# Kernel optimization log

Hardware: AMD Instinct MI355X
Metric: run time of the kernel (lower is better)

## Reference

```python
import jax, jax.numpy as jnp
import numpy as np

NUM_HEADS = 8
HEAD_DIM = 128
MAX_RES = 224.0


def rope_embed(feat_shape, dim, max_res=MAX_RES):
    # timm pixel_freq_bands: 2**linspace(0, log2(max_res)-1, dim//4) * pi
    num_bands = dim // 4
    bands = (2.0 ** jnp.linspace(0.0, float(np.log2(max_res)) - 1.0, num_bands)) * jnp.pi
    # pixel coords in [-1, 1] per spatial dim
    coords = [jnp.linspace(-1.0, 1.0, s) for s in feat_shape]
    grid = jnp.stack(jnp.meshgrid(*coords, indexing='ij'), axis=-1)[..., None]  # [H,W,2,1]
    pos = grid * bands  # [H,W,2,num_bands]
    n = int(np.prod(feat_shape))
    sin = jnp.repeat(jnp.sin(pos).reshape(n, -1), 2, axis=-1)  # [n, dim]
    cos = jnp.repeat(jnp.cos(pos).reshape(n, -1), 2, axis=-1)  # [n, dim]
    return sin, cos


def _rot(x):
    # interleaved rotate-half: (x0,x1,x2,x3,...) -> (-x1,x0,-x3,x2,...)
    return jnp.stack([-x[..., 1::2], x[..., ::2]], axis=-1).reshape(x.shape)


def setup_inputs() -> dict:
    key = jax.random.key(0)
    k1, k2, k3, k4 = jax.random.split(key, 4)
    C, E = 1024, 1024
    x = jax.random.normal(k1, (64, C, 16, 16), dtype=jnp.float32)
    qkv_w = jax.random.normal(k2, (3 * E, C), dtype=jnp.float32) * (C ** -0.5)
    qkv_b = jnp.zeros((3 * E,), dtype=jnp.float32)
    proj_w = jax.random.normal(k3, (E, E), dtype=jnp.float32) * (E ** -0.5)
    proj_b = jax.random.normal(k4, (E,), dtype=jnp.float32) * 0.02
    return {"x": x, "qkv_w": qkv_w, "qkv_b": qkv_b, "proj_w": proj_w, "proj_b": proj_b}


def reference(x, qkv_w, qkv_b, proj_w, proj_b):
    B, C, H, W = x.shape
    n = H * W
    scale = HEAD_DIM ** -0.5
    sin_emb, cos_emb = rope_embed((H, W), HEAD_DIM)  # [n, head_dim]

    t = x.reshape(B, C, n).transpose(0, 2, 1)                      # [B, n, C]
    t = jnp.concatenate([t.mean(axis=1, keepdims=True), t], axis=1)  # [B, n+1, C]

    qkv = t @ qkv_w.T + qkv_b                                      # [B, n+1, 3E]
    qkv = qkv.reshape(B, n + 1, 3, NUM_HEADS, HEAD_DIM).transpose(2, 0, 3, 1, 4)
    q, k, v = qkv[0], qkv[1], qkv[2]                               # [B, h, n+1, d]

    def apply_rope(z):
        zc, zs = z[:, :, :1], z[:, :, 1:]
        zs = zs * cos_emb + _rot(zs) * sin_emb
        return jnp.concatenate([zc, zs], axis=2)

    q = apply_rope(q)
    k = apply_rope(k)

    attn = jax.nn.softmax(jnp.einsum('bhqd,bhkd->bhqk', q, k) * scale, axis=-1)
    out = jnp.einsum('bhqk,bhkd->bhqd', attn, v)
    out = out.transpose(0, 2, 1, 3).reshape(B, n + 1, -1)           # [B, n+1, E]
    out = out @ proj_w.T + proj_b
    return out[:, 0]
```

## Files before the change

kernel.cpp:

```cpp
#include <hip/hip_runtime.h>
#include <math.h>

#define PI_F 3.14159265358979323846f
#define KSTEP 0.21959209425992272f

using bf16x8 = __attribute__((ext_vector_type(8))) short;
using f32x4 = __attribute__((ext_vector_type(4))) float;
using u16x8 = __attribute__((ext_vector_type(8))) unsigned short;

static __device__ __forceinline__ float wave_reduce_sum(float v) {
#pragma unroll
  for (int off = 32; off; off >>= 1) v += __shfl_down(v, off);
  return v;
}

static __device__ __forceinline__ unsigned short f2bf(float f) {
  unsigned u = __float_as_uint(f);
  return (unsigned short)((u + 0x7fffu + ((u >> 16) & 1u)) >> 16);
}

static __device__ __forceinline__ float bf2f(unsigned short s) {
  return __uint_as_float(((unsigned)s) << 16);
}

static __device__ __forceinline__ void gload_lds16(const void* g, void* l) {
  __builtin_amdgcn_global_load_lds((const __attribute__((address_space(1))) unsigned int*)g,
                                   (__attribute__((address_space(3))) unsigned int*)l, 16, 0, 0);
}

__global__ __launch_bounds__(256) void prep_kernel(const float* __restrict__ x,
                                                   const float* __restrict__ qkv_w,
                                                   unsigned short* __restrict__ xt,
                                                   float* __restrict__ t_mean,
                                                   unsigned short* __restrict__ wk_bf,
                                                   float2* __restrict__ sc) {
  const int bid = blockIdx.x;
  const int t = threadIdx.x;
  __shared__ float tile[64][33];
  if (bid < 1024) {
    const int ct = bid & 15, b = bid >> 4;
    const int cl = t >> 2, pq = (t & 3) * 8;
    const int pl = t >> 3, cq = (t & 7) * 8;
    float sum = 0.0f;
    const float* xrow = x + ((size_t)(b * 1024 + ct * 64 + cl) * 256) + pq;
    unsigned short* xtb = xt + (size_t)b * 262144 + ct * 64;
    for (int pt = 0; pt < 8; ++pt) {
      const float4 v0 = *reinterpret_cast<const float4*>(xrow + pt * 32);
      const float4 v1 = *reinterpret_cast<const float4*>(xrow + pt * 32 + 4);
      tile[cl][pq + 0] = v0.x; tile[cl][pq + 1] = v0.y; tile[cl][pq + 2] = v0.z; tile[cl][pq + 3] = v0.w;
      tile[cl][pq + 4] = v1.x; tile[cl][pq + 5] = v1.y; tile[cl][pq + 6] = v1.z; tile[cl][pq + 7] = v1.w;
      sum += (v0.x + v0.y) + (v0.z + v0.w) + (v1.x + v1.y) + (v1.z + v1.w);
      __syncthreads();
      u16x8 o;
#pragma unroll
      for (int e = 0; e < 8; ++e) o[e] = f2bf(tile[cq + e][pl]);
      *reinterpret_cast<u16x8*>(xtb + (size_t)(pt * 32 + pl) * 1024 + cq) = o;
      __syncthreads();
    }
    sum += __shfl_xor(sum, 1);
    sum += __shfl_xor(sum, 2);
    if ((t & 3) == 0) t_mean[b * 1024 + ct * 64 + cl] = sum * (1.0f / 256.0f);
  } else if (bid < 2048) {
    const int i = ((bid - 1024) * 256 + t) * 4;
    const float4 v = *reinterpret_cast<const float4*>(qkv_w + 1048576 + i);
    ushort4 r;
    r.x = f2bf(v.x); r.y = f2bf(v.y); r.z = f2bf(v.z); r.w = f2bf(v.w);
    *reinterpret_cast<ushort4*>(wk_bf + i) = r;
  } else {
    const int idx = (bid - 2048) * 256 + t;
    const int m = idx >> 8, j = idx & 255;
    const float band = exp2f((float)(m & 31) * KSTEP) * PI_F;
    const float coord = (m < 32) ? (-1.0f + (2.0f / 15.0f) * (float)(j >> 4))
                                 : (-1.0f + (2.0f / 15.0f) * (float)(j & 15));
    float sn, cs;
    sincosf(coord * band, &sn, &cs);
    sc[idx] = make_float2(sn, cs);
  }
}

__global__ __launch_bounds__(256) void gemm_splitk(
    const float* __restrict__ A, int lda, int aStrideZ,
    const float* __restrict__ B, int ldb, int bStrideZ,
    float* __restrict__ Cp, int ldc, int cStrideZ, int cStrideKc, int KC) {
  const int nt = blockIdx.x, mt = blockIdx.y;
  const int z = blockIdx.z / KC, kc = blockIdx.z % KC;
  const int tid = threadIdx.x;
  A += (size_t)z * aStrideZ + (size_t)mt * 32 * lda + kc * 256;
  B += (size_t)z * bStrideZ + (size_t)nt * 64 * ldb + kc * 256;
  Cp += (size_t)kc * cStrideKc + (size_t)z * cStrideZ + (size_t)mt * 32 * ldc + nt * 64;

  __shared__ float As[32][34];
  __shared__ float Bs[32][68];

  const int tm = tid >> 4;
  const int tn = tid & 15;
  float acc0[4] = {0, 0, 0, 0}, acc1[4] = {0, 0, 0, 0};

  for (int k0 = 0; k0 < 256; k0 += 32) {
    {
      const int m = tid >> 3, kq = tid & 7;
      float4 v = *reinterpret_cast<const float4*>(A + (size_t)m * lda + k0 + kq * 4);
      As[kq * 4 + 0][m] = v.x; As[kq * 4 + 1][m] = v.y;
      As[kq * 4 + 2][m] = v.z; As[kq * 4 + 3][m] = v.w;
    }
#pragma unroll
    for (int r = 0; r < 2; ++r) {
      const int idx = r * 256 + tid;
      const int n = idx >> 3, kq = idx & 7;
      float4 v = *reinterpret_cast<const float4*>(B + (size_t)n * ldb + k0 + kq * 4);
      Bs[kq * 4 + 0][n] = v.x; Bs[kq * 4 + 1][n] = v.y;
      Bs[kq * 4 + 2][n] = v.z; Bs[kq * 4 + 3][n] = v.w;
    }
    __syncthreads();
#pragma unroll
    for (int k = 0; k < 32; ++k) {
      const float a0 = As[k][tm * 2], a1 = As[k][tm * 2 + 1];
      const float4 bb = *reinterpret_cast<const float4*>(&Bs[k][tn * 4]);
      acc0[0] += a0 * bb.x; acc0[1] += a0 * bb.y; acc0[2] += a0 * bb.z; acc0[3] += a0 * bb.w;
      acc1[0] += a1 * bb.x; acc1[1] += a1 * bb.y; acc1[2] += a1 * bb.z; acc1[3] += a1 * bb.w;
    }
    __syncthreads();
  }
  *reinterpret_cast<float4*>(Cp + (size_t)(tm * 2) * ldc + tn * 4) =
      make_float4(acc0[0], acc0[1], acc0[2], acc0[3]);
  *reinterpret_cast<float4*>(Cp + (size_t)(tm * 2 + 1) * ldc + tn * 4) =
      make_float4(acc1[0], acc1[1], acc1[2], acc1[3]);
}

__global__ __launch_bounds__(256) void gemm_proj_splitk(
    const float* __restrict__ Apart, const float* __restrict__ abias,
    const float* __restrict__ B, float* __restrict__ Cp) {
  const int nt = blockIdx.x, mt = blockIdx.y, kc = blockIdx.z;
  const int tid = threadIdx.x;
  B += (size_t)nt * 64 * 1024 + kc * 256;
  Cp += (size_t)kc * 65536 + (size_t)mt * 32 * 1024 + nt * 64;

  __shared__ float As[32][34];
  __shared__ float Bs[32][68];

  const int tm = tid >> 4;
  const int tn = tid & 15;
  float acc0[4] = {0, 0, 0, 0}, acc1[4] = {0, 0, 0, 0};

  for (int k0 = 0; k0 < 256; k0 += 32) {
    {
      const int m = tid >> 3, kq = tid & 7;
      const int kg = kc * 256 + k0 + kq * 4;
      const float* Ab = Apart + (size_t)(mt * 32 + m) * 1024 + kg;
      float4 v = *reinterpret_cast<const float4*>(abias + kg);
#pragma unroll
      for (int r = 0; r < 4; ++r) {
        const float4 p = *reinterpret_cast<const float4*>(Ab + (size_t)r * 65536);
        v.x += p.x; v.y += p.y; v.z += p.z; v.w += p.w;
      }
      As[kq * 4 + 0][m] = v.x; As[kq * 4 + 1][m] = v.y;
      As[kq * 4 + 2][m] = v.z; As[kq * 4 + 3][m] = v.w;
    }
#pragma unroll
    for (int r = 0; r < 2; ++r) {
      const int idx = r * 256 + tid;
      const int n = idx >> 3, kq = idx & 7;
      float4 v = *reinterpret_cast<const float4*>(B + (size_t)n * 1024 + k0 + kq * 4);
      Bs[kq * 4 + 0][n] = v.x; Bs[kq * 4 + 1][n] = v.y;
      Bs[kq * 4 + 2][n] = v.z; Bs[kq * 4 + 3][n] = v.w;
    }
    __syncthreads();
#pragma unroll
    for (int k = 0; k < 32; ++k) {
      const float a0 = As[k][tm * 2], a1 = As[k][tm * 2 + 1];
      const float4 bb = *reinterpret_cast<const float4*>(&Bs[k][tn * 4]);
      acc0[0] += a0 * bb.x; acc0[1] += a0 * bb.y; acc0[2] += a0 * bb.z; acc0[3] += a0 * bb.w;
      acc1[0] += a1 * bb.x; acc1[1] += a1 * bb.y; acc1[2] += a1 * bb.z; acc1[3] += a1 * bb.w;
    }
    __syncthreads();
  }
  *reinterpret_cast<float4*>(Cp + (size_t)(tm * 2) * 1024 + tn * 4) =
      make_float4(acc0[0], acc0[1], acc0[2], acc0[3]);
  *reinterpret_cast<float4*>(Cp + (size_t)(tm * 2 + 1) * 1024 + tn * 4) =
      make_float4(acc1[0], acc1[1], acc1[2], acc1[3]);
}

__global__ __launch_bounds__(256) void reduce4_bias(const float* __restrict__ part,
                                                    const float* __restrict__ bias,
                                                    float* __restrict__ out) {
  const int i = blockIdx.x * 256 + threadIdx.x;
  out[i] = part[i] + part[i + 65536] + part[i + 131072] + part[i + 196608] + bias[i & 1023];
}

__global__ __launch_bounds__(512) void k_scores_mfma(
    const unsigned short* __restrict__ wk, const unsigned short* __restrict__ xt,
    const float* __restrict__ qkv_b, const float* __restrict__ q0p,
    const float2* __restrict__ sc, float* __restrict__ S) {
  const int l = blockIdx.x;
  const int b = ((l >> 7) << 3) + (l & 7);
  const int h = (l >> 4) & 7;
  const int jt = (l >> 3) & 1;
  const int tid = threadIdx.x;
  const int w = tid >> 6, lane = tid & 63;
  const int wm = (w >> 2) * 64, wn = (w & 3) * 32;

  __shared__ __align__(16) char smem[65536];

  const int rowA = lane >> 3, ci = lane & 7;
  const unsigned short* wkh = wk + (size_t)h * 128 * 1024;
  const unsigned short* xtb = xt + (size_t)b * 262144 + (size_t)jt * 128 * 1024;

  f32x4 acc[4][2] = {};

#define STAGE(sel, c0)                                                                   \
  {                                                                                      \
    char* Ab = smem + (sel)*32768;                                                       \
    char* Bb = Ab + 16384;                                                               \
    _Pragma("unroll") for (int i = 0; i < 2; ++i) {                                      \
      const int r = (w * 2 + i) * 8 + rowA;                                              \
      gload_lds16(wkh + (size_t)r * 1024 + (c0) + ((ci ^ (r & 7)) * 8),                  \
                  Ab + (w * 2 + i) * 1024);                                              \
      gload_lds16(xtb + (size_t)r * 1024 + (c0) + ((ci ^ (r & 7)) * 8),                  \
                  Bb + (w * 2 + i) * 1024);                                              \
    }                                                                                    \
  }

  STAGE(0, 0);
  __syncthreads();
  int cur = 0;
  for (int kt = 0; kt < 16; ++kt) {
    if (kt < 15) STAGE(cur ^ 1, (kt + 1) * 64);
    const char* Ab = smem + cur * 32768;
    const char* Bb = Ab + 16384;
#pragma unroll
    for (int kk = 0; kk < 2; ++kk) {
      const int coff = kk * 64 + (lane >> 4) * 16;
      bf16x8 af[4], bfr[2];
#pragma unroll
      for (int mi = 0; mi < 4; ++mi) {
        const int d = wm + mi * 16 + (lane & 15);
        af[mi] = *reinterpret_cast<const bf16x8*>(Ab + d * 128 + (coff ^ ((d & 7) << 4)));
      }
#pragma unroll
      for (int ni = 0; ni < 2; ++ni) {
        const int j = wn + ni * 16 + (lane & 15);
        bfr[ni] = *reinterpret_cast<const bf16x8*>(Bb + j * 128 + (coff ^ ((j & 7) << 4)));
      }
#pragma unroll
      for (int mi = 0; mi < 4; ++mi)
#pragma unroll
        for (int ni = 0; ni < 2; ++ni)
          acc[mi][ni] = __builtin_amdgcn_mfma_f32_16x16x32_bf16(af[mi], bfr[ni], acc[mi][ni], 0, 0, 0);
    }
    __syncthreads();
    cur ^= 1;
  }
#undef STAGE

  float* q0_lds = reinterpret_cast<float*>(smem + 57344);
  if (tid < 128) {
    const float* qp = q0p + (size_t)b * 2048 + h * 128 + tid;
    q0_lds[tid] = qkv_b[h * 128 + tid] + qp[0] + qp[131072] + qp[262144] + qp[393216];
  }
  __syncthreads();

  const float* bk = qkv_b + 1024 + h * 128;
  const int colj = lane & 15, rgrp = lane >> 4;
  float partial[2] = {0, 0};
#pragma unroll
  for (int mi = 0; mi < 4; ++mi) {
#pragma unroll
    for (int pp = 0; pp < 2; ++pp) {
      const int d0 = wm + mi * 16 + rgrp * 4 + pp * 2;
      const int m = d0 >> 1;
      const float2 qv = *reinterpret_cast<const float2*>(q0_lds + d0);
      const float2 bv = *reinterpret_cast<const float2*>(bk + d0);
#pragma unroll
      for (int ni = 0; ni < 2; ++ni) {
        const int j = jt * 128 + wn + ni * 16 + colj;
        const float ke = acc[mi][ni][pp * 2] + bv.x;
        const float ko = acc[mi][ni][pp * 2 + 1] + bv.y;
        const float2 t = sc[m * 256 + j];
        const float P = ke * qv.x + ko * qv.y;
        const float Q = ke * qv.y - ko * qv.x;
        partial[ni] += t.y * P + t.x * Q;
      }
    }
  }
  float* red = reinterpret_cast<float*>(smem);
#pragma unroll
  for (int ni = 0; ni < 2; ++ni)
    red[(wn + ni * 16 + colj) * 9 + (w >> 2) * 4 + rgrp] = partial[ni];
  __syncthreads();
  if (tid < 128) {
    float s = 0.0f;
#pragma unroll
    for (int k = 0; k < 8; ++k) s += red[tid * 9 + k];
    S[(size_t)(b * 8 + h) * 257 + 1 + jt * 128 + tid] = s;
  }
}

__global__ __launch_bounds__(64) void softmax_kernel(const float* __restrict__ q0p,
                                                     const float* __restrict__ qkv_b,
                                                     const float* __restrict__ S,
                                                     float* __restrict__ attn) {
  const int bh = blockIdx.x;
  const int b = bh >> 3, h = bh & 7;
  const int l = threadIdx.x;
  const float scale = 0.08838834764831845f;
  float q0a = qkv_b[h * 128 + l], q0b = qkv_b[h * 128 + l + 64];
  float k0a = qkv_b[1024 + h * 128 + l], k0b = qkv_b[1024 + h * 128 + l + 64];
  const float* base = q0p + (size_t)b * 2048;
#pragma unroll
  for (int kc = 0; kc < 4; ++kc) {
    const float* pp = base + (size_t)kc * 131072;
    q0a += pp[h * 128 + l];
    q0b += pp[h * 128 + l + 64];
    k0a += pp[1024 + h * 128 + l];
    k0b += pp[1024 + h * 128 + l + 64];
  }
  float p = q0a * k0a + q0b * k0b;
  p = wave_reduce_sum(p);
  const float s0 = __shfl(p, 0);
  const float* Sb = S + (size_t)bh * 257;
  float v[5];
  float mx = -3.0e38f;
  int cnt = 0;
  for (int j = l; j < 257; j += 64) {
    const float s = ((j == 0) ? s0 : Sb[j]) * scale;
    v[cnt++] = s;
    mx = fmaxf(mx, s);
  }
#pragma unroll
  for (int off = 32; off; off >>= 1) mx = fmaxf(mx, __shfl_xor(mx, off));
  float sum = 0.0f;
  for (int i = 0; i < cnt; ++i) {
    v[i] = expf(v[i] - mx);
    sum += v[i];
  }
#pragma unroll
  for (int off = 32; off; off >>= 1) sum += __shfl_xor(sum, off);
  const float inv = 1.0f / sum;
  int i = 0;
  for (int j = l; j < 257; j += 64) attn[(size_t)bh * 257 + j] = v[i++] * inv;
}

__global__ __launch_bounds__(256) void u_accum_kernel(const unsigned short* __restrict__ xt,
                                                      const float* __restrict__ t_mean,
                                                      const float* __restrict__ attn,
                                                      float* __restrict__ u) {
  const int ct = blockIdx.x;
  const int b = blockIdx.y;
  const int tid = threadIdx.x;
  __shared__ float aw[2056];
  __shared__ float red[8192];
  for (int i = tid; i < 2056; i += 256) aw[i] = attn[(size_t)(b * 8 + (i & 7)) * 257 + (i >> 3)];
  __syncthreads();
  const int cl = tid & 31, q = tid >> 5;
  const int c = ct * 128 + cl * 4;
  const unsigned short* xr = xt + (size_t)b * 262144 + c;
  float acc[8][4] = {};
  for (int p = q * 32; p < q * 32 + 32; ++p) {
    const ushort4 v = *reinterpret_cast<const ushort4*>(xr + (size_t)p * 1024);
    const float xs[4] = {bf2f(v.x), bf2f(v.y), bf2f(v.z), bf2f(v.w)};
    const float* w8 = &aw[(p + 1) * 8];
#pragma unroll
    for (int hh = 0; hh < 8; ++hh)
#pragma unroll
      for (int e = 0; e < 4; ++e) acc[hh][e] += w8[hh] * xs[e];
  }
#pragma unroll
  for (int hh = 0; hh < 8; ++hh)
#pragma unroll
    for (int e = 0; e < 4; ++e) red[q * 1024 + (cl * 8 + hh) * 4 + e] = acc[hh][e];
  __syncthreads();
#pragma unroll
  for (int r = 0; r < 4; ++r) {
    const int o = tid * 4 + r;
    const int cl2 = o >> 5, hh = (o >> 2) & 7, e = o & 3;
    float s = 0.0f;
#pragma unroll
    for (int qq = 0; qq < 8; ++qq) s += red[qq * 1024 + o];
    const int cc = ct * 128 + cl2 * 4 + e;
    s += aw[hh] * t_mean[b * 1024 + cc];
    u[(size_t)(b * 8 + hh) * 1024 + cc] = s;
  }
}

extern "C" void kernel_launch(void* const* d_in, const int* in_sizes, int n_in,
                              void* d_out, int out_size, void* d_ws, size_t ws_size,
                              hipStream_t stream) {
  const float* x = (const float*)d_in[0];
  const float* qkv_w = (const float*)d_in[1];
  const float* qkv_b = (const float*)d_in[2];
  const float* proj_w = (const float*)d_in[3];
  const float* proj_b = (const float*)d_in[4];
  float* out = (float*)d_out;

  float* ws = (float*)d_ws;
  float* t_mean = ws;
  float* q0k0_part = ws + 65536;
  float* S = ws + 589824;
  float* attn = ws + 721408;
  float* u = ws + 852992;
  float* out0_part = ws + 1377280;
  float* out_part = ws + 1639424;
  float2* sc = (float2*)(ws + 1901568);
  unsigned short* wk_bf = (unsigned short*)(ws + 1934336);
  unsigned short* x_t = (unsigned short*)(ws + 2458624);

  prep_kernel<<<2112, 256, 0, stream>>>(x, qkv_w, x_t, t_mean, wk_bf, sc);

  gemm_splitk<<<dim3(32, 2, 4), 256, 0, stream>>>(t_mean, 1024, 0, qkv_w, 1024, 0,
                                                  q0k0_part, 2048, 0, 131072, 4);

  k_scores_mfma<<<1024, 512, 0, stream>>>(wk_bf, x_t, qkv_b, q0k0_part, sc, S);

  softmax_kernel<<<512, 64, 0, stream>>>(q0k0_part, qkv_b, S, attn);

  u_accum_kernel<<<dim3(8, 64), 256, 0, stream>>>(x_t, t_mean, attn, u);

  gemm_splitk<<<dim3(2, 2, 32), 256, 0, stream>>>(u, 8192, 1024,
                                                  qkv_w + (size_t)2048 * 1024, 1024, 131072,
                                                  out0_part, 1024, 128, 65536, 4);

  gemm_proj_splitk<<<dim3(16, 2, 4), 256, 0, stream>>>(out0_part, qkv_b + 2048, proj_w, out_part);

  reduce4_bias<<<256, 256, 0, stream>>>(out_part, proj_b, out);
}
```

Baseline: 114.0 us.

## Fuse softmax into enlarged 256x256 k-scores MFMA tile with 4-stage pipeline

The k-scores GEMM now has each block compute a 256x256 tile covering two heads and all 256 keys, instead of a 128x128 tile per head and key-half. It uses a 4-deep LDS ring of gload_lds stages with vmcnt-based waits and s_setprio around the MFMA bursts. Because each block now holds full score rows, the softmax (including the CLS q0·k0 term) is computed in-block and attn is written directly, removing the separate softmax launch and the S round-trip through memory. The cost is 128KB of LDS, a grid of only 256 blocks at one block per CU, and more accumulator registers.

```diff
diff --git a/kernel.cpp b/kernel.cpp
--- a/kernel.cpp
+++ b/kernel.cpp
@@ -187,157 +187,164 @@
   out[i] = part[i] + part[i + 65536] + part[i + 131072] + part[i + 196608] + bias[i & 1023];
 }
 
-__global__ __launch_bounds__(512) void k_scores_mfma(
+__global__ __launch_bounds__(512, 1) void k_scores_mfma(
     const unsigned short* __restrict__ wk, const unsigned short* __restrict__ xt,
     const float* __restrict__ qkv_b, const float* __restrict__ q0p,
-    const float2* __restrict__ sc, float* __restrict__ S) {
+    const float2* __restrict__ sc, float* __restrict__ attn) {
   const int l = blockIdx.x;
-  const int b = ((l >> 7) << 3) + (l & 7);
-  const int h = (l >> 4) & 7;
-  const int jt = (l >> 3) & 1;
+  const int b = ((l >> 5) << 3) | (l & 7);
+  const int mt = (l >> 3) & 3;
   const int tid = threadIdx.x;
   const int w = tid >> 6, lane = tid & 63;
-  const int wm = (w >> 2) * 64, wn = (w & 3) * 32;
-
-  __shared__ __align__(16) char smem[65536];
-
-  const int rowA = lane >> 3, ci = lane & 7;
-  const unsigned short* wkh = wk + (size_t)h * 128 * 1024;
-  const unsigned short* xtb = xt + (size_t)b * 262144 + (size_t)jt * 128 * 1024;
-
-  f32x4 acc[4][2] = {};
-
-#define STAGE(sel, c0)                                                                   \
-  {                                                                                      \
-    char* Ab = smem + (sel)*32768;                                                       \
-    char* Bb = Ab + 16384;                                                               \
-    _Pragma("unroll") for (int i = 0; i < 2; ++i) {                                      \
-      const int r = (w * 2 + i) * 8 + rowA;                                              \
-      gload_lds16(wkh + (size_t)r * 1024 + (c0) + ((ci ^ (r & 7)) * 8),                  \
-                  Ab + (w * 2 + i) * 1024);                                              \
-      gload_lds16(xtb + (size_t)r * 1024 + (c0) + ((ci ^ (r & 7)) * 8),                  \
-                  Bb + (w * 2 + i) * 1024);                                              \
-    }                                                                                    \
-  }
-
-  STAGE(0, 0);
-  __syncthreads();
-  int cur = 0;
-  for (int kt = 0; kt < 16; ++kt) {
-    if (kt < 15) STAGE(cur ^ 1, (kt + 1) * 64);
-    const char* Ab = smem + cur * 32768;
+  const int wr = w >> 2, wc = w & 3;
+
+  __shared__ __align__(16) char smem[131072];
+
+  const unsigned short* wkA = wk + (size_t)(mt * 256) * 1024;
+  const unsigned short* xtb = xt + (size_t)b * 262144;
+
+  f32x4 acc[8][4] = {};
+
+#define STAGE4(tt, src)                                                          \
+  {                                                                              \
+    char* base_ = smem + ((tt)&3) * 32768;                                       \
+    const int c0_ = (src)*32;                                                    \
+    _Pragma("unroll") for (int c = 0; c < 2; ++c) {                              \
+      const int rb_ = w * 2 + c;                                                 \
+      const int row_ = rb_ * 16 + (lane >> 2);                                   \
+      const int sl_ = ((lane & 3) ^ ((row_ >> 1) & 3)) * 8;                      \
+      gload_lds16(wkA + (size_t)row_ * 1024 + c0_ + sl_, base_ + rb_ * 1024);    \
+      gload_lds16(xtb + (size_t)row_ * 1024 + c0_ + sl_,                         \
+                  base_ + 16384 + rb_ * 1024);                                   \
+    }                                                                            \
+  }
+
+  STAGE4(0, 0);
+  STAGE4(1, 1);
+  STAGE4(2, 2);
+
+  for (int t = 0; t < 32; ++t) {
+    {
+      const int tt = t + 3;
+      const int src = tt > 31 ? 31 : tt;
+      STAGE4(tt, src);
+    }
+    asm volatile("s_waitcnt vmcnt(12)" ::: "memory");
+    __builtin_amdgcn_s_barrier();
+    const char* Ab = smem + (t & 3) * 32768;
     const char* Bb = Ab + 16384;
-#pragma unroll
-    for (int kk = 0; kk < 2; ++kk) {
-      const int coff = kk * 64 + (lane >> 4) * 16;
-      bf16x8 af[4], bfr[2];
-#pragma unroll
-      for (int mi = 0; mi < 4; ++mi) {
-        const int d = wm + mi * 16 + (lane & 15);
-        af[mi] = *reinterpret_cast<const bf16x8*>(Ab + d * 128 + (coff ^ ((d & 7) << 4)));
+    bf16x8 bfrag[4];
+#pragma unroll
+    for (int ni = 0; ni < 4; ++ni) {
+      const int row = wc * 64 + ni * 16 + (lane & 15);
+      bfrag[ni] = *reinterpret_cast<const bf16x8*>(
+          Bb + row * 64 + (((lane >> 4) ^ ((row >> 1) & 3)) << 4));
+    }
+#pragma unroll
+    for (int mh = 0; mh < 2; ++mh) {
+      bf16x8 af[4];
+#pragma unroll
+      for (int q = 0; q < 4; ++q) {
+        const int row = wr * 128 + (mh * 4 + q) * 16 + (lane & 15);
+        af[q] = *reinterpret_cast<const bf16x8*>(
+            Ab + row * 64 + (((lane >> 4) ^ ((row >> 1) & 3)) << 4));
       }
-#pragma unroll
-      for (int ni = 0; ni < 2; ++ni) {
-        const int j = wn + ni * 16 + (lane & 15);
-        bfr[ni] = *reinterpret_cast<const bf16x8*>(Bb + j * 128 + (coff ^ ((j & 7) << 4)));
-      }
-#pragma unroll
-      for (int mi = 0; mi < 4; ++mi)
-#pragma unroll
-        for (int ni = 0; ni < 2; ++ni)
-          acc[mi][ni] = __builtin_amdgcn_mfma_f32_16x16x32_bf16(af[mi], bfr[ni], acc[mi][ni], 0, 0, 0);
-    }
-    __syncthreads();
-    cur ^= 1;
-  }
-#undef STAGE
-
-  float* q0_lds = reinterpret_cast<float*>(smem + 57344);
-  if (tid < 128) {
-    const float* qp = q0p + (size_t)b * 2048 + h * 128 + tid;
-    q0_lds[tid] = qkv_b[h * 128 + tid] + qp[0] + qp[131072] + qp[262144] + qp[393216];
-  }
-  __syncthreads();
-
-  const float* bk = qkv_b + 1024 + h * 128;
+      __builtin_amdgcn_s_setprio(1);
+#pragma unroll
+      for (int q = 0; q < 4; ++q)
+#pragma unroll
+        for (int ni = 0; ni < 4; ++ni)
+          acc[mh * 4 + q][ni] = __builtin_amdgcn_mfma_f32_16x16x32_bf16(
+              af[q], bfrag[ni], acc[mh * 4 + q][ni], 0, 0, 0);
+      __builtin_amdgcn_s_setprio(0);
+    }
+    __builtin_amdgcn_s_barrier();
+    asm volatile("" ::: "memory");
+  }
+#undef STAGE4
+
+  asm volatile("s_waitcnt vmcnt(0)" ::: "memory");
+  __syncthreads();
+
+  float* q0_lds = reinterpret_cast<float*>(smem);
+  float* k0_lds = q0_lds + 256;
+  float* Sh = k0_lds + 256;
+  float* ps = Sh + 520;
+  float* r4 = ps + 4;
+
+  if (tid < 256) {
+    const float* qp = q0p + (size_t)b * 2048 + mt * 256 + tid;
+    q0_lds[tid] = qkv_b[mt * 256 + tid] + qp[0] + qp[131072] + qp[262144] + qp[393216];
+    const float* kp = qp + 1024;
+    k0_lds[tid] = qkv_b[1024 + mt * 256 + tid] + kp[0] + kp[131072] + kp[262144] + kp[393216];
+  }
+  __syncthreads();
+
+  if (tid < 256) {
+    float pr = q0_lds[tid] * k0_lds[tid];
+    pr = wave_reduce_sum(pr);
+    if (lane == 0) ps[tid >> 6] = pr;
+  }
+
   const int colj = lane & 15, rgrp = lane >> 4;
-  float partial[2] = {0, 0};
-#pragma unroll
-  for (int mi = 0; mi < 4; ++mi) {
+  const float* bk = qkv_b + 1024 + mt * 256 + wr * 128;
+  float partial[4] = {0, 0, 0, 0};
+#pragma unroll
+  for (int mi = 0; mi < 8; ++mi) {
 #pragma unroll
     for (int pp = 0; pp < 2; ++pp) {
-      const int d0 = wm + mi * 16 + rgrp * 4 + pp * 2;
-      const int m = d0 >> 1;
-      const float2 qv = *reinterpret_cast<const float2*>(q0_lds + d0);
-      const float2 bv = *reinterpret_cast<const float2*>(bk + d0);
-#pragma unroll
-      for (int ni = 0; ni < 2; ++ni) {
-        const int j = jt * 128 + wn + ni * 16 + colj;
+      const int dd = mi * 16 + rgrp * 4 + pp * 2;
+      const int m = dd >> 1;
+      const float2 qv = *reinterpret_cast<const float2*>(q0_lds + wr * 128 + dd);
+      const float2 bv = *reinterpret_cast<const float2*>(bk + dd);
+#pragma unroll
+      for (int ni = 0; ni < 4; ++ni) {
+        const int j = wc * 64 + ni * 16 + colj;
         const float ke = acc[mi][ni][pp * 2] + bv.x;
         const float ko = acc[mi][ni][pp * 2 + 1] + bv.y;
-        const float2 t = sc[m * 256 + j];
-        const float P = ke * qv.x + ko * qv.y;
-        const float Q = ke * qv.y - ko * qv.x;
-        partial[ni] += t.y * P + t.x * Q;
+        const float2 tt = sc[m * 256 + j];
+        partial[ni] += tt.y * (ke * qv.x + ko * qv.y) + tt.x * (ke * qv.y - ko * qv.x);
       }
     }
   }
-  float* red = reinterpret_cast<float*>(smem);
-#pragma unroll
-  for (int ni = 0; ni < 2; ++ni)
-    red[(wn + ni * 16 + colj) * 9 + (w >> 2) * 4 + rgrp] = partial[ni];
-  __syncthreads();
-  if (tid < 128) {
-    float s = 0.0f;
-#pragma unroll
-    for (int k = 0; k < 8; ++k) s += red[tid * 9 + k];
-    S[(size_t)(b * 8 + h) * 257 + 1 + jt * 128 + tid] = s;
-  }
-}
-
-__global__ __launch_bounds__(64) void softmax_kernel(const float* __restrict__ q0p,
-                                                     const float* __restrict__ qkv_b,
-                                                     const float* __restrict__ S,
-                                                     float* __restrict__ attn) {
-  const int bh = blockIdx.x;
-  const int b = bh >> 3, h = bh & 7;
-  const int l = threadIdx.x;
+#pragma unroll
+  for (int ni = 0; ni < 4; ++ni) {
+    partial[ni] += __shfl_xor(partial[ni], 16);
+    partial[ni] += __shfl_xor(partial[ni], 32);
+  }
+  if (lane < 16) {
+#pragma unroll
+    for (int ni = 0; ni < 4; ++ni)
+      Sh[wr * 260 + 1 + wc * 64 + ni * 16 + colj] = partial[ni];
+  }
+  __syncthreads();
+  if (tid == 0) { Sh[0] = ps[0] + ps[1]; Sh[260] = ps[2] + ps[3]; }
+  __syncthreads();
+
+  const int hg = tid >> 8, i = tid & 255;
   const float scale = 0.08838834764831845f;
-  float q0a = qkv_b[h * 128 + l], q0b = qkv_b[h * 128 + l + 64];
-  float k0a = qkv_b[1024 + h * 128 + l], k0b = qkv_b[1024 + h * 128 + l + 64];
-  const float* base = q0p + (size_t)b * 2048;
-#pragma unroll
-  for (int kc = 0; kc < 4; ++kc) {
-    const float* pp = base + (size_t)kc * 131072;
-    q0a += pp[h * 128 + l];
-    q0b += pp[h * 128 + l + 64];
-    k0a += pp[1024 + h * 128 + l];
-    k0b += pp[1024 + h * 128 + l + 64];
-  }
-  float p = q0a * k0a + q0b * k0b;
-  p = wave_reduce_sum(p);
-  const float s0 = __shfl(p, 0);
-  const float* Sb = S + (size_t)bh * 257;
-  float v[5];
-  float mx = -3.0e38f;
-  int cnt = 0;
-  for (int j = l; j < 257; j += 64) {
-    const float s = ((j == 0) ? s0 : Sb[j]) * scale;
-    v[cnt++] = s;
-    mx = fmaxf(mx, s);
-  }
+  const float* Sr = Sh + hg * 260;
+  const float va = Sr[i] * scale;
+  const float vb = (i == 0) ? Sr[256] * scale : -3.0e38f;
+  float mx = fmaxf(va, vb);
 #pragma unroll
   for (int off = 32; off; off >>= 1) mx = fmaxf(mx, __shfl_xor(mx, off));
-  float sum = 0.0f;
-  for (int i = 0; i < cnt; ++i) {
-    v[i] = expf(v[i] - mx);
-    sum += v[i];
-  }
+  if (lane == 0) r4[hg * 4 + ((tid >> 6) & 3)] = mx;
+  __syncthreads();
+  mx = fmaxf(fmaxf(r4[hg * 4], r4[hg * 4 + 1]), fmaxf(r4[hg * 4 + 2], r4[hg * 4 + 3]));
+  const float ea = expf(va - mx);
+  const float eb = (i == 0) ? expf(vb - mx) : 0.0f;
+  float sum = ea + eb;
 #pragma unroll
   for (int off = 32; off; off >>= 1) sum += __shfl_xor(sum, off);
+  __syncthreads();
+  if (lane == 0) r4[hg * 4 + ((tid >> 6) & 3)] = sum;
+  __syncthreads();
+  sum = r4[hg * 4] + r4[hg * 4 + 1] + r4[hg * 4 + 2] + r4[hg * 4 + 3];
   const float inv = 1.0f / sum;
-  int i = 0;
-  for (int j = l; j < 257; j += 64) attn[(size_t)bh * 257 + j] = v[i++] * inv;
+  float* ab = attn + (size_t)(b * 8 + 2 * mt + hg) * 257;
+  ab[i] = ea * inv;
+  if (i == 0) ab[256] = eb * inv;
 }
 
 __global__ __launch_bounds__(256) void u_accum_kernel(const unsigned short* __restrict__ xt,
@@ -395,7 +402,6 @@
   float* ws = (float*)d_ws;
   float* t_mean = ws;
   float* q0k0_part = ws + 65536;
-  float* S = ws + 589824;
   float* attn = ws + 721408;
   float* u = ws + 852992;
   float* out0_part = ws + 1377280;
@@ -409,9 +415,7 @@
   gemm_splitk<<<dim3(32, 2, 4), 256, 0, stream>>>(t_mean, 1024, 0, qkv_w, 1024, 0,
                                                   q0k0_part, 2048, 0, 131072, 4);
 
-  k_scores_mfma<<<1024, 512, 0, stream>>>(wk_bf, x_t, qkv_b, q0k0_part, sc, S);
-
-  softmax_kernel<<<512, 64, 0, stream>>>(q0k0_part, qkv_b, S, attn);
+  k_scores_mfma<<<256, 512, 0, stream>>>(wk_bf, x_t, qkv_b, q0k0_part, sc, attn);
 
   u_accum_kernel<<<dim3(8, 64), 256, 0, stream>>>(x_t, t_mean, attn, u);
 
```

New measurement: 110.1 us. 3.5% less time.
